# Optimization experiments

Measured on AMD Instinct MI355X. Metric: run time of the kernel, lower is better.

## Reference

```python
import jax, jax.numpy as jnp
import numpy as np

B, C_IN, C_OUT, H, W, K = 8, 32, 32, 96, 96, 5


def setup_inputs() -> dict:
    key = jax.random.key(0)
    k1, k2 = jax.random.split(key)
    f = jax.random.normal(k1, (B, C_IN, H, W), dtype=jnp.float32)
    # xavier_uniform-style init for the structuring element h
    fan_in = C_IN * K * K
    fan_out = C_OUT * K * K
    bound = float(np.sqrt(6.0 / (fan_in + fan_out)))
    h = jax.random.uniform(k2, (C_OUT, C_IN, K, K), dtype=jnp.float32,
                           minval=-bound, maxval=bound)
    return {"f": f, "h": h}


def reference(f, h):
    """Morphological max-plus dilation with 'same' padding.

    out[b,o,y,x] = max_{c,i,j} f[b,c,y+i-p, x+j-p] + h[o,c,i,j]
    """
    b, c, hh, ww = f.shape
    o, _, k, _ = h.shape
    p = k // 2
    neg = -jnp.finfo(f.dtype).max / 2
    fp = jnp.pad(f, ((0, 0), (0, 0), (p, p), (p, p)), constant_values=neg)
    out = jnp.full((b, o, hh, ww), neg, dtype=f.dtype)
    for i in range(k):          # fixed small kernel loop (k*k = 25 taps)
        for j in range(k):
            sl = fp[:, :, i:i + hh, j:j + ww]              # (B, C, H, W)
            w_ij = h[:, :, i, j]                            # (O, C)
            # max-plus over input channels: (B,1,C,H,W) + (O,C,1,1)
            cand = jnp.max(sl[:, None] + w_ij[None, :, :, None, None], axis=2)
            out = jnp.maximum(out, cand)
    return out
```

## Files before the change

### kernel.cpp

```cpp
#include <hip/hip_runtime.h>
#include <hip/hip_fp16.h>


#define B_ 8
#define C_ 32
#define O_ 32
#define H_ 96
#define W_ 96
#define K_ 5

#define TX_ 24
#define RY_ 8
#define CS_ 2
#define TY_ (RY_ * CS_)
#define NT_ (TX_ * TY_)
#define XR_ 4
#define OP_ 2
#define OB_ (OP_ * 2)
#define CG_ (C_ / CS_)

#define PH_ 100
#define PW_ 104

#define NEGF (-30000.0f)

typedef _Float16 h2 __attribute__((ext_vector_type(2)));

static __device__ __forceinline__ h2 h2_from_bits(unsigned u) {
    return __builtin_bit_cast(h2, u);
}
static __device__ __forceinline__ unsigned bits_from_h2(h2 v) {
    return __builtin_bit_cast(unsigned, v);
}

__global__ __launch_bounds__(256)
void prepad_kernel(const float* __restrict__ f, unsigned* __restrict__ fpad) {
    const int idx = blockIdx.x * 256 + threadIdx.x;
    const int c = blockIdx.y;
    const int b = blockIdx.z;
    if (idx >= PH_ * PW_) return;
    const int row = idx / PW_;
    const int col = idx - row * PW_;
    const int y = row - 2;
    const int x = col - 2;
    float v = NEGF;
    if ((unsigned)y < H_ && (unsigned)x < W_)
        v = f[((size_t)(b * C_ + c) * H_ + y) * W_ + x];
    _Float16 hv = (_Float16)v;
    h2 d; d.x = hv; d.y = hv;
    fpad[((size_t)(b * C_ + c) * PH_ + row) * PW_ + col] = bits_from_h2(d);
}

template <bool PADDED>
__global__ __launch_bounds__(NT_)
void dilate_main(const unsigned* __restrict__ fpad, const float* __restrict__ f,
                 const float* __restrict__ h, float* __restrict__ out) {
    const int tx  = threadIdx.x;
    const int ty  = threadIdx.y;
    const int tid = ty * TX_ + tx;
    const int g   = ty >> 3;
    const int r   = ty & 7;
    const int t192 = r * TX_ + tx;

    const int ytile = blockIdx.x;
    const int og    = blockIdx.y;
    const int b     = blockIdx.z;
    const int y0 = ytile * RY_;
    const int o0 = og * OB_;
    const int x0 = XR_ * tx;

    __shared__ unsigned hs[C_][K_][K_][OP_];
    __shared__ unsigned comb[OP_ * XR_][RY_ * TX_];
    for (int idx = tid; idx < C_ * K_ * K_ * OP_; idx += NT_) {
        int c  = idx / (K_ * K_ * OP_);
        int rr = idx - c * (K_ * K_ * OP_);
        int ij = rr / OP_;
        int op = rr - ij * OP_;
        int o  = o0 + 2 * op;
        float h0 = h[((size_t)o * C_ + c) * (K_ * K_) + ij];
        float h1 = h[((size_t)(o + 1) * C_ + c) * (K_ * K_) + ij];
        h2 p; p.x = (_Float16)h0; p.y = (_Float16)h1;
        hs[c][ij / K_][ij - (ij / K_) * K_][op] = bits_from_h2(p);
    }
    __syncthreads();

    h2 acc[OP_][XR_];
    {
        h2 neg; neg.x = (_Float16)NEGF; neg.y = (_Float16)NEGF;
#pragma unroll
        for (int op = 0; op < OP_; ++op)
#pragma unroll
            for (int xx = 0; xx < XR_; ++xx) acc[op][xx] = neg;
    }

    const int cbase = g * CG_;
    for (int cc = 0; cc < CG_; ++cc) {
        const int c = cbase + cc;
        h2 a[K_][8];
        if (PADDED) {
            const unsigned* fp = fpad + (size_t)(b * C_ + c) * (PH_ * PW_);
#pragma unroll
            for (int i = 0; i < K_; ++i) {
                const int row = y0 + r + i;
                const uint4* p = (const uint4*)(fp + row * PW_ + 4 * tx);
                uint4 w0 = p[0];
                uint4 w1 = p[1];
                a[i][0] = h2_from_bits(w0.x); a[i][1] = h2_from_bits(w0.y);
                a[i][2] = h2_from_bits(w0.z); a[i][3] = h2_from_bits(w0.w);
                a[i][4] = h2_from_bits(w1.x); a[i][5] = h2_from_bits(w1.y);
                a[i][6] = h2_from_bits(w1.z); a[i][7] = h2_from_bits(w1.w);
            }
        } else {
            const float* fc = f + (size_t)(b * C_ + c) * (H_ * W_);
#pragma unroll
            for (int i = 0; i < K_; ++i) {
                const int yy = y0 + r + i - 2;
                const bool yok = (unsigned)yy < H_;
                const float* frow = fc + (size_t)(yok ? yy : 0) * W_;
#pragma unroll
                for (int t = 0; t < 8; ++t) {
                    int xc = x0 - 2 + t;
                    bool ok = yok && ((unsigned)xc < W_);
                    float v = frow[ok ? xc : 0];
                    v = ok ? v : NEGF;
                    _Float16 hv = (_Float16)v;
                    h2 d; d.x = hv; d.y = hv;
                    a[i][t] = d;
                }
            }
        }

#pragma unroll
        for (int i = 0; i < K_; ++i) {
#pragma unroll
            for (int j = 0; j < K_; ++j) {
                uint2 hb = *(const uint2*)&hs[c][i][j][0];
                h2 h0 = h2_from_bits(hb.x);
                h2 h1 = h2_from_bits(hb.y);
#pragma unroll
                for (int xx = 0; xx < XR_; ++xx) {
                    h2 fv = a[i][xx + j];
                    acc[0][xx] = __builtin_elementwise_max(acc[0][xx], fv + h0);
                    acc[1][xx] = __builtin_elementwise_max(acc[1][xx], fv + h1);
                }
            }
        }
    }

    if (g == 1) {
#pragma unroll
        for (int op = 0; op < OP_; ++op)
#pragma unroll
            for (int xx = 0; xx < XR_; ++xx)
                comb[op * XR_ + xx][t192] = bits_from_h2(acc[op][xx]);
    }
    __syncthreads();
    if (g == 0) {
#pragma unroll
        for (int op = 0; op < OP_; ++op)
#pragma unroll
            for (int xx = 0; xx < XR_; ++xx) {
                h2 other = h2_from_bits(comb[op * XR_ + xx][t192]);
                acc[op][xx] = __builtin_elementwise_max(acc[op][xx], other);
            }

        const int y = y0 + r;
#pragma unroll
        for (int op = 0; op < OP_; ++op) {
            const int o = o0 + 2 * op;
            float4 lo = make_float4((float)acc[op][0].x, (float)acc[op][1].x,
                                    (float)acc[op][2].x, (float)acc[op][3].x);
            float4 hi = make_float4((float)acc[op][0].y, (float)acc[op][1].y,
                                    (float)acc[op][2].y, (float)acc[op][3].y);
            *(float4*)&out[(((size_t)b * O_ + o)     * H_ + y) * W_ + x0] = lo;
            *(float4*)&out[(((size_t)b * O_ + o + 1) * H_ + y) * W_ + x0] = hi;
        }
    }
}

extern "C" void kernel_launch(void* const* d_in, const int* in_sizes, int n_in,
                              void* d_out, int out_size, void* d_ws, size_t ws_size,
                              hipStream_t stream) {
    const float* f = (const float*)d_in[0];
    const float* h = (const float*)d_in[1];
    float* out = (float*)d_out;

    dim3 mgrid(H_ / RY_, O_ / OB_, B_);
    dim3 mblock(TX_, TY_);

    const size_t need = (size_t)B_ * C_ * PH_ * PW_ * sizeof(unsigned);
    if (ws_size >= need) {
        unsigned* fpad = (unsigned*)d_ws;
        dim3 pgrid((PH_ * PW_ + 255) / 256, C_, B_);
        hipLaunchKernelGGL(prepad_kernel, pgrid, dim3(256), 0, stream, f, fpad);
        hipLaunchKernelGGL((dilate_main<true>), mgrid, mblock, 0, stream,
                           fpad, f, h, out);
    } else {
        hipLaunchKernelGGL((dilate_main<false>), mgrid, mblock, 0, stream,
                           (const unsigned*)nullptr, f, h, out);
    }
}
```

Before: 146.7 us.

## Compute two output rows per thread and double-buffer channel windows

Each thread now computes two output rows (YR_=2) from a shared 6-row input window, so each loaded row and each h value read from shared memory serves more outputs. Blocks shrink to 192 threads covering the same 8-row tile. The channel loop is unrolled by two with ping-pong register windows, so the next channel's loads overlap the current channel's max-plus math. A min-blocks launch bound is added. Register pressure roughly doubles (accumulators plus two windows), which may limit occupancy or cause spills.

Result: slower. 213.4 us (+45.5%).

```diff
diff --git a/kernel.cpp b/kernel.cpp
--- a/kernel.cpp
+++ b/kernel.cpp
@@ -1,5 +1,4 @@
 #include <hip/hip_runtime.h>
-#include <hip/hip_fp16.h>
 
 
 #define B_ 8
@@ -10,26 +9,29 @@
 #define K_ 5
 
 #define TX_ 24
-#define RY_ 8
+#define RT_ 4
 #define CS_ 2
-#define TY_ (RY_ * CS_)
+#define TY_ (RT_ * CS_)
 #define NT_ (TX_ * TY_)
 #define XR_ 4
+#define YR_ 2
 #define OP_ 2
 #define OB_ (OP_ * 2)
 #define CG_ (C_ / CS_)
+#define WR_ (YR_ + K_ - 1)
 
 #define PH_ 100
 #define PW_ 104
+#define PLSZ_ (PH_ * PW_)
 
 #define NEGF (-30000.0f)
 
 typedef _Float16 h2 __attribute__((ext_vector_type(2)));
 
-static __device__ __forceinline__ h2 h2_from_bits(unsigned u) {
+static __device__ __forceinline__ h2 h2b(unsigned u) {
     return __builtin_bit_cast(h2, u);
 }
-static __device__ __forceinline__ unsigned bits_from_h2(h2 v) {
+static __device__ __forceinline__ unsigned bh2(h2 v) {
     return __builtin_bit_cast(unsigned, v);
 }
 
@@ -38,7 +40,7 @@
     const int idx = blockIdx.x * 256 + threadIdx.x;
     const int c = blockIdx.y;
     const int b = blockIdx.z;
-    if (idx >= PH_ * PW_) return;
+    if (idx >= PLSZ_) return;
     const int row = idx / PW_;
     const int col = idx - row * PW_;
     const int y = row - 2;
@@ -48,29 +50,85 @@
         v = f[((size_t)(b * C_ + c) * H_ + y) * W_ + x];
     _Float16 hv = (_Float16)v;
     h2 d; d.x = hv; d.y = hv;
-    fpad[((size_t)(b * C_ + c) * PH_ + row) * PW_ + col] = bits_from_h2(d);
+    fpad[(size_t)(b * C_ + c) * PLSZ_ + idx] = bh2(d);
+}
+
+__device__ __forceinline__ void load_win(const unsigned* __restrict__ base,
+                                         h2 w[WR_][8]) {
+#pragma unroll
+    for (int t = 0; t < WR_; ++t) {
+        const uint4* p = (const uint4*)(base + t * PW_);
+        uint4 a = p[0];
+        uint4 b = p[1];
+        w[t][0] = h2b(a.x); w[t][1] = h2b(a.y); w[t][2] = h2b(a.z); w[t][3] = h2b(a.w);
+        w[t][4] = h2b(b.x); w[t][5] = h2b(b.y); w[t][6] = h2b(b.z); w[t][7] = h2b(b.w);
+    }
+}
+
+__device__ __forceinline__ void load_win_direct(const float* __restrict__ fc,
+                                                int y0r, int x0, h2 w[WR_][8]) {
+#pragma unroll
+    for (int t = 0; t < WR_; ++t) {
+        const int yy = y0r + t - 2;
+        const bool yok = (unsigned)yy < H_;
+        const float* frow = fc + (size_t)(yok ? yy : 0) * W_;
+#pragma unroll
+        for (int q = 0; q < 8; ++q) {
+            int xc = x0 - 2 + q;
+            bool ok = yok && ((unsigned)xc < W_);
+            float v = frow[ok ? xc : 0];
+            v = ok ? v : NEGF;
+            _Float16 hv = (_Float16)v;
+            h2 d; d.x = hv; d.y = hv;
+            w[t][q] = d;
+        }
+    }
+}
+
+__device__ __forceinline__ void do_math(const unsigned hsrow[K_][K_][OP_],
+                                        const h2 w[WR_][8],
+                                        h2 acc[YR_][OP_][XR_]) {
+#pragma unroll
+    for (int i = 0; i < K_; ++i) {
+#pragma unroll
+        for (int j = 0; j < K_; ++j) {
+            uint2 hb = *(const uint2*)&hsrow[i][j][0];
+            h2 h0 = h2b(hb.x);
+            h2 h1 = h2b(hb.y);
+#pragma unroll
+            for (int xx = 0; xx < XR_; ++xx) {
+                h2 f0 = w[i][xx + j];
+                acc[0][0][xx] = __builtin_elementwise_max(acc[0][0][xx], f0 + h0);
+                acc[0][1][xx] = __builtin_elementwise_max(acc[0][1][xx], f0 + h1);
+                h2 f1 = w[i + 1][xx + j];
+                acc[1][0][xx] = __builtin_elementwise_max(acc[1][0][xx], f1 + h0);
+                acc[1][1][xx] = __builtin_elementwise_max(acc[1][1][xx], f1 + h1);
+            }
+        }
+    }
 }
 
 template <bool PADDED>
-__global__ __launch_bounds__(NT_)
+__global__ __launch_bounds__(NT_, 3)
 void dilate_main(const unsigned* __restrict__ fpad, const float* __restrict__ f,
                  const float* __restrict__ h, float* __restrict__ out) {
     const int tx  = threadIdx.x;
     const int ty  = threadIdx.y;
     const int tid = ty * TX_ + tx;
-    const int g   = ty >> 3;
-    const int r   = ty & 7;
-    const int t192 = r * TX_ + tx;
+    const int ry  = ty & (RT_ - 1);
+    const int g   = ty >> 2;
 
     const int ytile = blockIdx.x;
     const int og    = blockIdx.y;
     const int b     = blockIdx.z;
-    const int y0 = ytile * RY_;
+    const int y0 = ytile * (RT_ * YR_);
     const int o0 = og * OB_;
     const int x0 = XR_ * tx;
+    const int yb = y0 + YR_ * ry;
 
     __shared__ unsigned hs[C_][K_][K_][OP_];
-    __shared__ unsigned comb[OP_ * XR_][RY_ * TX_];
+    __shared__ unsigned comb[YR_ * OP_ * XR_][RT_ * TX_];
+
     for (int idx = tid; idx < C_ * K_ * K_ * OP_; idx += NT_) {
         int c  = idx / (K_ * K_ * OP_);
         int rr = idx - c * (K_ * K_ * OP_);
@@ -80,100 +138,81 @@
         float h0 = h[((size_t)o * C_ + c) * (K_ * K_) + ij];
         float h1 = h[((size_t)(o + 1) * C_ + c) * (K_ * K_) + ij];
         h2 p; p.x = (_Float16)h0; p.y = (_Float16)h1;
-        hs[c][ij / K_][ij - (ij / K_) * K_][op] = bits_from_h2(p);
+        hs[c][ij / K_][ij - (ij / K_) * K_][op] = bh2(p);
     }
     __syncthreads();
 
-    h2 acc[OP_][XR_];
+    h2 acc[YR_][OP_][XR_];
     {
         h2 neg; neg.x = (_Float16)NEGF; neg.y = (_Float16)NEGF;
 #pragma unroll
-        for (int op = 0; op < OP_; ++op)
-#pragma unroll
-            for (int xx = 0; xx < XR_; ++xx) acc[op][xx] = neg;
-    }
-
-    const int cbase = g * CG_;
-    for (int cc = 0; cc < CG_; ++cc) {
-        const int c = cbase + cc;
-        h2 a[K_][8];
-        if (PADDED) {
-            const unsigned* fp = fpad + (size_t)(b * C_ + c) * (PH_ * PW_);
-#pragma unroll
-            for (int i = 0; i < K_; ++i) {
-                const int row = y0 + r + i;
-                const uint4* p = (const uint4*)(fp + row * PW_ + 4 * tx);
-                uint4 w0 = p[0];
-                uint4 w1 = p[1];
-                a[i][0] = h2_from_bits(w0.x); a[i][1] = h2_from_bits(w0.y);
-                a[i][2] = h2_from_bits(w0.z); a[i][3] = h2_from_bits(w0.w);
-                a[i][4] = h2_from_bits(w1.x); a[i][5] = h2_from_bits(w1.y);
-                a[i][6] = h2_from_bits(w1.z); a[i][7] = h2_from_bits(w1.w);
-            }
-        } else {
-            const float* fc = f + (size_t)(b * C_ + c) * (H_ * W_);
-#pragma unroll
-            for (int i = 0; i < K_; ++i) {
-                const int yy = y0 + r + i - 2;
-                const bool yok = (unsigned)yy < H_;
-                const float* frow = fc + (size_t)(yok ? yy : 0) * W_;
-#pragma unroll
-                for (int t = 0; t < 8; ++t) {
-                    int xc = x0 - 2 + t;
-                    bool ok = yok && ((unsigned)xc < W_);
-                    float v = frow[ok ? xc : 0];
-                    v = ok ? v : NEGF;
-                    _Float16 hv = (_Float16)v;
-                    h2 d; d.x = hv; d.y = hv;
-                    a[i][t] = d;
-                }
-            }
-        }
-
-#pragma unroll
-        for (int i = 0; i < K_; ++i) {
-#pragma unroll
-            for (int j = 0; j < K_; ++j) {
-                uint2 hb = *(const uint2*)&hs[c][i][j][0];
-                h2 h0 = h2_from_bits(hb.x);
-                h2 h1 = h2_from_bits(hb.y);
-#pragma unroll
-                for (int xx = 0; xx < XR_; ++xx) {
-                    h2 fv = a[i][xx + j];
-                    acc[0][xx] = __builtin_elementwise_max(acc[0][xx], fv + h0);
-                    acc[1][xx] = __builtin_elementwise_max(acc[1][xx], fv + h1);
-                }
-            }
-        }
-    }
-
+        for (int r = 0; r < YR_; ++r)
+#pragma unroll
+            for (int op = 0; op < OP_; ++op)
+#pragma unroll
+                for (int xx = 0; xx < XR_; ++xx) acc[r][op][xx] = neg;
+    }
+
+    const int c0 = g * CG_;
+    h2 wA[WR_][8], wB[WR_][8];
+
+    if (PADDED) {
+        const unsigned* p = fpad + (size_t)(b * C_ + c0) * PLSZ_ + yb * PW_ + x0;
+        load_win(p, wA);
+        for (int cc = 0; cc < CG_; cc += 2) {
+            load_win(p + (size_t)(cc + 1) * PLSZ_, wB);
+            do_math(hs[c0 + cc], wA, acc);
+            if (cc + 2 < CG_) load_win(p + (size_t)(cc + 2) * PLSZ_, wA);
+            do_math(hs[c0 + cc + 1], wB, acc);
+        }
+    } else {
+        const float* fb = f + (size_t)(b * C_ + c0) * (H_ * W_);
+        load_win_direct(fb, yb, x0, wA);
+        for (int cc = 0; cc < CG_; cc += 2) {
+            load_win_direct(fb + (size_t)(cc + 1) * (H_ * W_), yb, x0, wB);
+            do_math(hs[c0 + cc], wA, acc);
+            if (cc + 2 < CG_)
+                load_win_direct(fb + (size_t)(cc + 2) * (H_ * W_), yb, x0, wA);
+            do_math(hs[c0 + cc + 1], wB, acc);
+        }
+    }
+
+    const int t96 = ry * TX_ + tx;
     if (g == 1) {
 #pragma unroll
-        for (int op = 0; op < OP_; ++op)
-#pragma unroll
-            for (int xx = 0; xx < XR_; ++xx)
-                comb[op * XR_ + xx][t192] = bits_from_h2(acc[op][xx]);
+        for (int r = 0; r < YR_; ++r)
+#pragma unroll
+            for (int op = 0; op < OP_; ++op)
+#pragma unroll
+                for (int xx = 0; xx < XR_; ++xx)
+                    comb[(r * OP_ + op) * XR_ + xx][t96] = bh2(acc[r][op][xx]);
     }
     __syncthreads();
     if (g == 0) {
 #pragma unroll
-        for (int op = 0; op < OP_; ++op)
-#pragma unroll
-            for (int xx = 0; xx < XR_; ++xx) {
-                h2 other = h2_from_bits(comb[op * XR_ + xx][t192]);
-                acc[op][xx] = __builtin_elementwise_max(acc[op][xx], other);
+        for (int r = 0; r < YR_; ++r)
+#pragma unroll
+            for (int op = 0; op < OP_; ++op)
+#pragma unroll
+                for (int xx = 0; xx < XR_; ++xx) {
+                    h2 other = h2b(comb[(r * OP_ + op) * XR_ + xx][t96]);
+                    acc[r][op][xx] =
+                        __builtin_elementwise_max(acc[r][op][xx], other);
+                }
+
+#pragma unroll
+        for (int r = 0; r < YR_; ++r) {
+            const int y = yb + r;
+#pragma unroll
+            for (int op = 0; op < OP_; ++op) {
+                const int o = o0 + 2 * op;
+                float4 lo = make_float4((float)acc[r][op][0].x, (float)acc[r][op][1].x,
+                                        (float)acc[r][op][2].x, (float)acc[r][op][3].x);
+                float4 hi = make_float4((float)acc[r][op][0].y, (float)acc[r][op][1].y,
+                                        (float)acc[r][op][2].y, (float)acc[r][op][3].y);
+                *(float4*)&out[(((size_t)b * O_ + o)     * H_ + y) * W_ + x0] = lo;
+                *(float4*)&out[(((size_t)b * O_ + o + 1) * H_ + y) * W_ + x0] = hi;
             }
-
-        const int y = y0 + r;
-#pragma unroll
-        for (int op = 0; op < OP_; ++op) {
-            const int o = o0 + 2 * op;
-            float4 lo = make_float4((float)acc[op][0].x, (float)acc[op][1].x,
-                                    (float)acc[op][2].x, (float)acc[op][3].x);
-            float4 hi = make_float4((float)acc[op][0].y, (float)acc[op][1].y,
-                                    (float)acc[op][2].y, (float)acc[op][3].y);
-            *(float4*)&out[(((size_t)b * O_ + o)     * H_ + y) * W_ + x0] = lo;
-            *(float4*)&out[(((size_t)b * O_ + o + 1) * H_ + y) * W_ + x0] = hi;
         }
     }
 }
@@ -185,13 +224,13 @@
     const float* h = (const float*)d_in[1];
     float* out = (float*)d_out;
 
-    dim3 mgrid(H_ / RY_, O_ / OB_, B_);
+    dim3 mgrid(H_ / (RT_ * YR_), O_ / OB_, B_);
     dim3 mblock(TX_, TY_);
 
-    const size_t need = (size_t)B_ * C_ * PH_ * PW_ * sizeof(unsigned);
+    const size_t need = (size_t)B_ * C_ * PLSZ_ * sizeof(unsigned);
     if (ws_size >= need) {
         unsigned* fpad = (unsigned*)d_ws;
-        dim3 pgrid((PH_ * PW_ + 255) / 256, C_, B_);
+        dim3 pgrid((PLSZ_ + 255) / 256, C_, B_);
         hipLaunchKernelGGL(prepad_kernel, pgrid, dim3(256), 0, stream, f, fpad);
         hipLaunchKernelGGL((dilate_main<true>), mgrid, mblock, 0, stream,
                            fpad, f, h, out);
```
